# Kernel optimization log

Hardware: AMD Instinct MI355X
Metric: run time of the kernel (lower is better)

Reference implementation:

```python
import jax, jax.numpy as jnp
import numpy as np

K = 3          # spline order
NUM = 32       # grid intervals G
IN_DIM = 256
OUT_DIM = 512
BATCH = 2048


def _b_spline_basis(x, grid, k):
    """Cox-de-Boor recursion. x: (B, I); grid: (I, G+2k+1) -> (B, I, G+k)."""
    xg = x[:, :, None]                      # (B, I, 1)
    g = grid[None, :, :]                    # (1, I, G+2k+1)
    val = ((xg >= g[:, :, :-1]) & (xg < g[:, :, 1:])).astype(x.dtype)
    for p in range(1, k + 1):
        left = (xg - g[:, :, :-(p + 1)]) / (g[:, :, p:-1] - g[:, :, :-(p + 1)])
        right = (g[:, :, p + 1:] - xg) / (g[:, :, p + 1:] - g[:, :, 1:-p])
        val = left * val[:, :, :-1] + right * val[:, :, 1:]
    return val                               # (B, I, G+k)


def setup_inputs() -> dict:
    key = jax.random.key(0)
    k1, k2, k3 = jax.random.split(key, 3)
    x = jax.random.normal(k1, (BATCH, IN_DIM), dtype=jnp.float32)
    # uniform grid on [-1, 1], extended by k knots on each side (extend_grid)
    base = np.linspace(-1.0, 1.0, NUM + 1)
    h = 2.0 / NUM
    ext = np.concatenate([base[0] - h * np.arange(K, 0, -1), base,
                          base[-1] + h * np.arange(1, K + 1)]).astype(np.float32)
    grid = jnp.tile(jnp.asarray(ext)[None, :], (IN_DIM, 1))  # (I, G+2k+1)
    coef = 0.1 * jax.random.normal(k2, (IN_DIM, OUT_DIM, NUM + K), dtype=jnp.float32)
    scale_base = jax.random.normal(k3, (IN_DIM, OUT_DIM), dtype=jnp.float32) / np.sqrt(IN_DIM).astype(np.float32)
    scale_sp = jnp.ones((IN_DIM, OUT_DIM), dtype=jnp.float32) / np.sqrt(IN_DIM).astype(np.float32)
    mask = jnp.ones((IN_DIM, OUT_DIM), dtype=jnp.float32)
    return {"x": x, "grid": grid, "coef": coef,
            "scale_base": scale_base, "scale_sp": scale_sp, "mask": mask}


def reference(x, grid, coef, scale_base, scale_sp, mask):
    base = jax.nn.silu(x)                                   # b(x) residual, (B, I)
    bases = _b_spline_basis(x, grid, K)                     # (B, I, G+k)
    # coef2curve: einsum('ijk,jlk->ijl') in pykan -> (B, I, O)
    y = jnp.einsum('bik,iok->bio', bases, coef)
    y = scale_base[None, :, :] * base[:, :, None] + scale_sp[None, :, :] * y
    y = mask[None, :, :] * y
    return jnp.sum(y, axis=1)                               # (B, O)
```

## Files before the change

### kernel.cpp

```cpp
#include <hip/hip_runtime.h>
#include <math.h>

#define BATCH   2048
#define IN_DIM  256
#define OUT_DIM 512
#define NK      35
#define KS      48
#define KG      6
#define BTILE   128
#define OTILE   128
#define ICHUNK  16
#define NSPLIT  16
#define NBUF    2
#define COEFS_BYTES ((size_t)IN_DIM * OUT_DIM * KS * 2)
#define PART_ELEMS  ((size_t)BATCH * OUT_DIM)

__device__ __forceinline__ unsigned short f2bf(float x) {
    unsigned u = __float_as_uint(x);
    u += 0x7FFF + ((u >> 16) & 1);
    return (unsigned short)(u >> 16);
}
__device__ __forceinline__ float bf2f(unsigned short h) {
    return __uint_as_float(((unsigned)h) << 16);
}
__device__ __forceinline__ unsigned pack2(unsigned short a, unsigned short b) {
    return (unsigned)a | ((unsigned)b << 16);
}

typedef __bf16 bf16x8 __attribute__((ext_vector_type(8)));
typedef float  f32x16 __attribute__((ext_vector_type(16)));
typedef int    i32x4  __attribute__((ext_vector_type(4)));
typedef unsigned int u32;

__device__ __forceinline__ void gload_lds16(const void* g, void* l) {
    __builtin_amdgcn_global_load_lds((const __attribute__((address_space(1))) u32*)g,
                                     (__attribute__((address_space(3))) u32*)l, 16, 0, 0);
}

__device__ __forceinline__ unsigned lds_off(const void* p) {
    return (unsigned)(uintptr_t)(const __attribute__((address_space(3))) char*)p;
}

__device__ __forceinline__ i32x4 ds_read128(unsigned base, int off) {
    i32x4 r;
    asm volatile("ds_read_b128 %0, %1 offset:%c2"
                 : "=v"(r) : "v"(base), "i"(off));
    return r;
}
__device__ __forceinline__ bf16x8 as_bf16x8(i32x4 v) {
    bf16x8 r; __builtin_memcpy(&r, &v, 16); return r;
}

#define PR 32
__global__ __launch_bounds__(256) void kan_prep(
    const float* __restrict__ coef,
    const float* __restrict__ scale_base,
    const float* __restrict__ scale_sp,
    const float* __restrict__ mask,
    unsigned short* __restrict__ coefS)
{
    __shared__ float sc[PR * NK];
    __shared__ float sspm[PR], ssbm[PR];
    const int t    = threadIdx.x;
    const int row0 = blockIdx.x * PR;

    {
        const float4* csrc = (const float4*)(coef + (size_t)row0 * NK);
        float4* cdst = (float4*)sc;
        cdst[t] = csrc[t];
        if (t < 24) cdst[t + 256] = csrc[t + 256];
    }
    if (t < PR) {
        float m = mask[row0 + t];
        sspm[t] = scale_sp[row0 + t] * m;
        ssbm[t] = scale_base[row0 + t] * m;
    }
    __syncthreads();

    if (t < PR * 6) {
        int r = t / 6;
        int q = t - r * 6;
        float spm = sspm[r];
        const float* c = sc + r * NK;
        uint4 v = make_uint4(0u, 0u, 0u, 0u);
        if (q < 4) {
            const float* cq = c + q * 8;
            v.x = pack2(f2bf(cq[0] * spm), f2bf(cq[1] * spm));
            v.y = pack2(f2bf(cq[2] * spm), f2bf(cq[3] * spm));
            v.z = pack2(f2bf(cq[4] * spm), f2bf(cq[5] * spm));
            v.w = pack2(f2bf(cq[6] * spm), f2bf(cq[7] * spm));
        } else if (q == 4) {
            float sbm = ssbm[r];
            unsigned short hi = f2bf(sbm);
            unsigned short lo = f2bf(sbm - bf2f(hi));
            v.x = pack2(f2bf(c[32] * spm), f2bf(c[33] * spm));
            v.y = pack2(f2bf(c[34] * spm), 0);
            v.z = pack2(hi, hi);
            v.w = pack2(lo, 0);
        }
        int g = row0 + r;
        size_t di = ((size_t)(((g >> 9) * 4 + ((g >> 7) & 3)) * 6 + q)) * 128
                  + (size_t)(g & 127);
        ((uint4*)coefS)[di] = v;
    }
}

__global__ __launch_bounds__(256, 3) void kan_mfma(
    const float* __restrict__ x,
    const unsigned short* __restrict__ coefS,
    float* __restrict__ part)
{
    __shared__ __align__(16) short sA[2 * BTILE * KS];
    __shared__ __align__(16) short sB[NBUF * OTILE * KS];

    const int t    = threadIdx.x;
    const int w    = t >> 6;
    const int lane = t & 63;
    const int l31  = lane & 31, lh = lane >> 5;
    const int wr   = w & 1;
    const int wc   = w >> 1;
    const int o0   = blockIdx.x * OTILE;
    const int b0   = blockIdx.y * BTILE;
    const int ic0  = blockIdx.z * ICHUNK;
    const bool bTh = (t >= 128);
    const int wbase = t & 64;

    {
        uint4 z = make_uint4(0, 0, 0, 0);
        #pragma unroll
        for (int u = 0; u < 6; ++u) {
            int idx = t + 256 * u;
            if (idx < (2 * BTILE * KS * 2) / 16) ((uint4*)sA)[idx] = z;
        }
    }

    f32x16 acc00 = {}, acc01 = {}, acc10 = {}, acc11 = {};

    float xreg = 0.0f;
    int om0 = 0, om1 = 0;

    auto stageA = [&](short* abuf, int row, float xv, int& omn) {
        unsigned* rp = (unsigned*)abuf + row * 4;
        auto PADDR = [&](int p) -> unsigned* {
            return rp + (p >> 2) * (BTILE * 4) + (p & 3);
        };
        int oc = omn;
        *PADDR(oc)     = 0;
        *PADDR(oc + 1) = 0;
        *PADDR(oc + 2) = 0;

        float xn = (xv + 1.1875f) * 16.0f;
        float jf = floorf(xn);
        int   j  = (int)jf;
        float u  = xn - jf;
        bool valid = (xn >= 0.0f) && (j <= 37);
        float u2 = u * u, u3 = u2 * u;
        float w0 = (1.0f / 6.0f) * (1.0f - 3.0f * u + 3.0f * u2 - u3);
        float w1 = (1.0f / 6.0f) * (3.0f * u3 - 6.0f * u2 + 4.0f);
        float w2 = (1.0f / 6.0f) * (-3.0f * u3 + 3.0f * u2 + 3.0f * u + 1.0f);
        float w3 = (1.0f / 6.0f) * u3;
        int jb = j - 3;
        unsigned short h0 = f2bf(w0), h1 = f2bf(w1), h2 = f2bf(w2), h3 = f2bf(w3);
        int  m0  = jb >> 1;
        bool odd = (jb & 1) != 0;
        unsigned C0 = odd ? pack2(0, h0)
                          : (jb == 34 ? pack2(h0, 0) : pack2(h0, h1));
        unsigned C1 = odd ? (jb == 33 ? pack2(h1, 0) : pack2(h1, h2))
                          : (jb == 32 ? pack2(h2, 0) : pack2(h2, h3));
        unsigned C2 = pack2(h3, 0);
        if (valid) {
            if (m0 >= 0)                        *PADDR(m0)     = C0;
            if (m0 + 1 >= 0 && jb != 34)        *PADDR(m0 + 1) = C1;
            if (odd && jb != 33 && m0 + 2 >= 0) *PADDR(m0 + 2) = C2;
        }
        omn = min(max(m0, 0), 15);
        float sig = 1.0f / (1.0f + __expf(-xv));
        float s   = xv * sig;
        unsigned short shi = f2bf(s);
        unsigned short slo = f2bf(s - bf2f(shi));
        uint2 bw; bw.x = pack2(shi, slo); bw.y = pack2(shi, 0);
        *(uint2*)PADDR(18) = bw;
    };

    auto issueB = [&](int i, int buf) {
        const char* gsrc = (const char*)coefS
                         + ((size_t)i * 4 + (o0 >> 7)) * (KG * OTILE * 8 * 2);
        #pragma unroll
        for (int q = 0; q < 6; ++q) {
            int slot = wbase + (t & 63) + 128 * q;
            gload_lds16(gsrc + slot * 16,
                        (void*)(sB + buf * (OTILE * KS) + (wbase + 128 * q) * 8));
        }
    };

    __syncthreads();

    if (!bTh) {
        float x0 = x[(size_t)(b0 + t) * IN_DIM + ic0];
        stageA(sA, t, x0, om0);
        xreg = x[(size_t)(b0 + t) * IN_DIM + ic0 + 1];
    } else {
        issueB(ic0, 0);
    }
    if (bTh) asm volatile("s_waitcnt vmcnt(0)" ::: "memory");
    else     asm volatile("s_waitcnt lgkmcnt(0)" ::: "memory");
    __builtin_amdgcn_s_barrier();
    __builtin_amdgcn_sched_barrier(0);

    const unsigned sAoff = lds_off(sA);
    const unsigned sBoff = lds_off(sB);

    auto body = [&](int it, int& omn) {
        if (bTh && it + 1 < ICHUNK) issueB(ic0 + it + 1, (it + 1) & 1);

        const int cur = it & 1;
        const unsigned Abo = sAoff
            + (unsigned)(cur * (BTILE * KS) + (lh * BTILE + wr * 64 + l31) * 8) * 2u;
        const unsigned Bbo = sBoff
            + (unsigned)(cur * (OTILE * KS) + (lh * OTILE + wc * 64 + l31) * 8) * 2u;

        i32x4 a0r[3], a1r[3], b0r[3], b1r[3];
        #pragma unroll
        for (int s = 0; s < 3; ++s) {
            a0r[s] = ds_read128(Abo, s * 4096);
            a1r[s] = ds_read128(Abo, s * 4096 + 512);
            b0r[s] = ds_read128(Bbo, s * 4096);
            b1r[s] = ds_read128(Bbo, s * 4096 + 512);
        }

        if (!bTh && it + 1 < ICHUNK) {
            stageA(sA + ((it + 1) & 1) * (BTILE * KS), t, xreg, omn);
            if (it + 2 < ICHUNK)
                xreg = x[(size_t)(b0 + t) * IN_DIM + ic0 + it + 2];
        }

        asm volatile("s_waitcnt lgkmcnt(0)" ::: "memory");
        __builtin_amdgcn_sched_barrier(0);

        __builtin_amdgcn_s_setprio(1);
        #pragma unroll
        for (int s = 0; s < 3; ++s) {
            acc00 = __builtin_amdgcn_mfma_f32_32x32x16_bf16(as_bf16x8(a0r[s]), as_bf16x8(b0r[s]), acc00, 0, 0, 0);
            acc01 = __builtin_amdgcn_mfma_f32_32x32x16_bf16(as_bf16x8(a0r[s]), as_bf16x8(b1r[s]), acc01, 0, 0, 0);
            acc10 = __builtin_amdgcn_mfma_f32_32x32x16_bf16(as_bf16x8(a1r[s]), as_bf16x8(b0r[s]), acc10, 0, 0, 0);
            acc11 = __builtin_amdgcn_mfma_f32_32x32x16_bf16(as_bf16x8(a1r[s]), as_bf16x8(b1r[s]), acc11, 0, 0, 0);
        }
        __builtin_amdgcn_s_setprio(0);

        if (it + 1 < ICHUNK) {
            if (bTh) asm volatile("s_waitcnt vmcnt(0)" ::: "memory");
            __builtin_amdgcn_s_barrier();
            __builtin_amdgcn_sched_barrier(0);
        }
    };

    for (int itp = 0; itp < ICHUNK / 2; ++itp) {
        body(2 * itp,     om1);
        body(2 * itp + 1, om0);
    }

    __syncthreads();

    float* tp = (float*)sA + w * (32 * 36);
    float* pdst = part + (size_t)blockIdx.z * PART_ELEMS;
    #pragma unroll
    for (int r = 0; r < 2; ++r) {
        #pragma unroll
        for (int c = 0; c < 2; ++c) {
            const f32x16& acc = (r == 0) ? ((c == 0) ? acc00 : acc01)
                                         : ((c == 0) ? acc10 : acc11);
            #pragma unroll
            for (int reg = 0; reg < 16; ++reg) {
                int row = (reg & 3) + 8 * (reg >> 2) + 4 * lh;
                tp[row * 36 + l31] = acc[reg];
            }
            int cc = (lane & 7) * 4;
            #pragma unroll
            for (int j = 0; j < 4; ++j) {
                int rr = j * 8 + (lane >> 3);
                float4 v = *(float4*)&tp[rr * 36 + cc];
                int rowg = b0 + wr * 64 + r * 32 + rr;
                int colg = o0 + wc * 64 + c * 32 + cc;
                *(float4*)&pdst[(size_t)rowg * OUT_DIM + colg] = v;
            }
        }
    }
}

__global__ __launch_bounds__(256) void kan_reduce(
    const float4* __restrict__ part, float4* __restrict__ out)
{
    const size_t e = (size_t)blockIdx.x * 256 + threadIdx.x;
    float4 s = part[e];
    #pragma unroll
    for (int z = 1; z < NSPLIT; ++z) {
        float4 v = part[(size_t)z * (PART_ELEMS / 4) + e];
        s.x += v.x; s.y += v.y; s.z += v.z; s.w += v.w;
    }
    out[e] = s;
}

extern "C" void kernel_launch(void* const* d_in, const int* in_sizes, int n_in,
                              void* d_out, int out_size, void* d_ws, size_t ws_size,
                              hipStream_t stream) {
    const float* x          = (const float*)d_in[0];
    const float* coef       = (const float*)d_in[2];
    const float* scale_base = (const float*)d_in[3];
    const float* scale_sp   = (const float*)d_in[4];
    const float* mask       = (const float*)d_in[5];
    unsigned short* coefS   = (unsigned short*)d_ws;
    float* part             = (float*)((char*)d_ws + COEFS_BYTES);

    kan_prep<<<dim3(IN_DIM * OUT_DIM / PR), dim3(256), 0, stream>>>(
        coef, scale_base, scale_sp, mask, coefS);
    kan_mfma<<<dim3(OUT_DIM / OTILE, BATCH / BTILE, NSPLIT), dim3(256), 0, stream>>>(
        x, coefS, part);
    kan_reduce<<<dim3(BATCH * OUT_DIM / 4 / 256), dim3(256), 0, stream>>>(
        (const float4*)part, (float4*)d_out);
}
```

Baseline: 131.3 us.

## Precompute spline basis in prep kernel and deepen coef prefetch pipeline

Moves per-element B-spline weight and SiLU computation out of the MFMA kernel into the prep kernel, which writes packed basis words and bf16 hi/lo SiLU values to workspace. The MFMA kernel now only loads these and scatters them into LDS. It also raises the coefficient buffer count to four, prefetches three stages ahead with a partial vmcnt wait, and doubles the input-chunk length while halving the split count. In exchange it adds 24 bytes of workspace traffic per x element, uses more LDS, and lowers the occupancy bound from three to two blocks.

```diff
diff --git a/kernel.cpp b/kernel.cpp
--- a/kernel.cpp
+++ b/kernel.cpp
@@ -9,11 +9,13 @@
 #define KG      6
 #define BTILE   128
 #define OTILE   128
-#define ICHUNK  16
-#define NSPLIT  16
-#define NBUF    2
+#define ICHUNK  32
+#define NSPLIT  8
+#define NBUF    4
 #define COEFS_BYTES ((size_t)IN_DIM * OUT_DIM * KS * 2)
 #define PART_ELEMS  ((size_t)BATCH * OUT_DIM)
+#define XP4_OFF (COEFS_BYTES + (size_t)NSPLIT * PART_ELEMS * 4)
+#define XP2_OFF (XP4_OFF + (size_t)BATCH * IN_DIM * 16)
 
 __device__ __forceinline__ unsigned short f2bf(float x) {
     unsigned u = __float_as_uint(x);
@@ -53,11 +55,14 @@
 
 #define PR 32
 __global__ __launch_bounds__(256) void kan_prep(
+    const float* __restrict__ x,
     const float* __restrict__ coef,
     const float* __restrict__ scale_base,
     const float* __restrict__ scale_sp,
     const float* __restrict__ mask,
-    unsigned short* __restrict__ coefS)
+    unsigned short* __restrict__ coefS,
+    uint4* __restrict__ xp4,
+    uint2* __restrict__ xp2)
 {
     __shared__ float sc[PR * NK];
     __shared__ float sspm[PR], ssbm[PR];
@@ -74,6 +79,44 @@
         float m = mask[row0 + t];
         sspm[t] = scale_sp[row0 + t] * m;
         ssbm[t] = scale_base[row0 + t] * m;
+    }
+
+    if (blockIdx.x < (BATCH * IN_DIM) / 256) {
+        int flat = blockIdx.x * 256 + t;
+        float xv = x[flat];
+        float xn = (xv + 1.1875f) * 16.0f;
+        float jf = floorf(xn);
+        int   j  = (int)jf;
+        float u  = xn - jf;
+        bool valid = (xn >= 0.0f) && (j <= 37);
+        float u2 = u * u, u3 = u2 * u;
+        float w0 = (1.0f / 6.0f) * (1.0f - 3.0f * u + 3.0f * u2 - u3);
+        float w1 = (1.0f / 6.0f) * (3.0f * u3 - 6.0f * u2 + 4.0f);
+        float w2 = (1.0f / 6.0f) * (-3.0f * u3 + 3.0f * u2 + 3.0f * u + 1.0f);
+        float w3f = (1.0f / 6.0f) * u3;
+        int jb = j - 3;
+        unsigned short h0 = f2bf(w0), h1 = f2bf(w1), h2 = f2bf(w2), h3 = f2bf(w3f);
+        int  m0  = jb >> 1;
+        bool odd = (jb & 1) != 0;
+        unsigned C0 = odd ? pack2(0, h0)
+                          : (jb == 34 ? pack2(h0, 0) : pack2(h0, h1));
+        unsigned C1 = odd ? (jb == 33 ? pack2(h1, 0) : pack2(h1, h2))
+                          : (jb == 32 ? pack2(h2, 0) : pack2(h2, h3));
+        unsigned C2 = pack2(h3, 0);
+        int e0 = (valid && (m0 >= 0)) ? 1 : 0;
+        int e1 = (valid && (m0 + 1 >= 0) && (jb != 34)) ? 1 : 0;
+        int e2 = (valid && odd && (jb != 33) && (m0 + 2 >= 0)) ? 1 : 0;
+        int sat = min(max(m0, -2), 17);
+        uint4 c;
+        c.x = C0; c.y = C1; c.z = C2;
+        c.w = (unsigned)((sat + 2) | (e0 << 8) | (e1 << 9) | (e2 << 10));
+        float sig = 1.0f / (1.0f + __expf(-xv));
+        float s   = xv * sig;
+        unsigned short shi = f2bf(s);
+        unsigned short slo = f2bf(s - bf2f(shi));
+        uint2 bw; bw.x = pack2(shi, slo); bw.y = pack2(shi, 0);
+        xp4[flat] = c;
+        xp2[flat] = bw;
     }
     __syncthreads();
 
@@ -105,8 +148,10 @@
     }
 }
 
-__global__ __launch_bounds__(256, 3) void kan_mfma(
+__global__ __launch_bounds__(256, 2) void kan_mfma(
     const float* __restrict__ x,
+    const uint4* __restrict__ xp4,
+    const uint2* __restrict__ xp2,
     const unsigned short* __restrict__ coefS,
     float* __restrict__ part)
 {
@@ -136,10 +181,11 @@
 
     f32x16 acc00 = {}, acc01 = {}, acc10 = {}, acc11 = {};
 
-    float xreg = 0.0f;
     int om0 = 0, om1 = 0;
-
-    auto stageA = [&](short* abuf, int row, float xv, int& omn) {
+    uint4 cA = make_uint4(0, 0, 0, 0);
+    uint2 bA = make_uint2(0, 0);
+
+    auto stageA = [&](short* abuf, int row, uint4 c, uint2 bw, int& omn) {
         unsigned* rp = (unsigned*)abuf + row * 4;
         auto PADDR = [&](int p) -> unsigned* {
             return rp + (p >> 2) * (BTILE * 4) + (p & 3);
@@ -148,37 +194,12 @@
         *PADDR(oc)     = 0;
         *PADDR(oc + 1) = 0;
         *PADDR(oc + 2) = 0;
-
-        float xn = (xv + 1.1875f) * 16.0f;
-        float jf = floorf(xn);
-        int   j  = (int)jf;
-        float u  = xn - jf;
-        bool valid = (xn >= 0.0f) && (j <= 37);
-        float u2 = u * u, u3 = u2 * u;
-        float w0 = (1.0f / 6.0f) * (1.0f - 3.0f * u + 3.0f * u2 - u3);
-        float w1 = (1.0f / 6.0f) * (3.0f * u3 - 6.0f * u2 + 4.0f);
-        float w2 = (1.0f / 6.0f) * (-3.0f * u3 + 3.0f * u2 + 3.0f * u + 1.0f);
-        float w3 = (1.0f / 6.0f) * u3;
-        int jb = j - 3;
-        unsigned short h0 = f2bf(w0), h1 = f2bf(w1), h2 = f2bf(w2), h3 = f2bf(w3);
-        int  m0  = jb >> 1;
-        bool odd = (jb & 1) != 0;
-        unsigned C0 = odd ? pack2(0, h0)
-                          : (jb == 34 ? pack2(h0, 0) : pack2(h0, h1));
-        unsigned C1 = odd ? (jb == 33 ? pack2(h1, 0) : pack2(h1, h2))
-                          : (jb == 32 ? pack2(h2, 0) : pack2(h2, h3));
-        unsigned C2 = pack2(h3, 0);
-        if (valid) {
-            if (m0 >= 0)                        *PADDR(m0)     = C0;
-            if (m0 + 1 >= 0 && jb != 34)        *PADDR(m0 + 1) = C1;
-            if (odd && jb != 33 && m0 + 2 >= 0) *PADDR(m0 + 2) = C2;
-        }
+        int w3 = (int)c.w;
+        int m0 = (w3 & 255) - 2;
+        if (w3 & 256)  *PADDR(m0)     = c.x;
+        if (w3 & 512)  *PADDR(m0 + 1) = c.y;
+        if (w3 & 1024) *PADDR(m0 + 2) = c.z;
         omn = min(max(m0, 0), 15);
-        float sig = 1.0f / (1.0f + __expf(-xv));
-        float s   = xv * sig;
-        unsigned short shi = f2bf(s);
-        unsigned short slo = f2bf(s - bf2f(shi));
-        uint2 bw; bw.x = pack2(shi, slo); bw.y = pack2(shi, 0);
         *(uint2*)PADDR(18) = bw;
     };
 
@@ -196,13 +217,18 @@
     __syncthreads();
 
     if (!bTh) {
-        float x0 = x[(size_t)(b0 + t) * IN_DIM + ic0];
-        stageA(sA, t, x0, om0);
-        xreg = x[(size_t)(b0 + t) * IN_DIM + ic0 + 1];
+        size_t xbase = (size_t)(b0 + t) * IN_DIM + ic0;
+        uint4 c0 = xp4[xbase];
+        uint2 b0v = xp2[xbase];
+        stageA(sA, t, c0, b0v, om0);
+        cA = xp4[xbase + 1];
+        bA = xp2[xbase + 1];
     } else {
-        issueB(ic0, 0);
-    }
-    if (bTh) asm volatile("s_waitcnt vmcnt(0)" ::: "memory");
+        issueB(ic0,     0);
+        issueB(ic0 + 1, 1);
+        issueB(ic0 + 2, 2);
+    }
+    if (bTh) asm volatile("s_waitcnt vmcnt(12)" ::: "memory");
     else     asm volatile("s_waitcnt lgkmcnt(0)" ::: "memory");
     __builtin_amdgcn_s_barrier();
     __builtin_amdgcn_sched_barrier(0);
@@ -211,13 +237,17 @@
     const unsigned sBoff = lds_off(sB);
 
     auto body = [&](int it, int& omn) {
-        if (bTh && it + 1 < ICHUNK) issueB(ic0 + it + 1, (it + 1) & 1);
+        if (bTh && it + 1 < ICHUNK) {
+            int ip3 = (it + 3 < ICHUNK) ? (it + 3) : (ICHUNK - 1);
+            issueB(ic0 + ip3, (it + 3) & (NBUF - 1));
+        }
 
         const int cur = it & 1;
         const unsigned Abo = sAoff
             + (unsigned)(cur * (BTILE * KS) + (lh * BTILE + wr * 64 + l31) * 8) * 2u;
         const unsigned Bbo = sBoff
-            + (unsigned)(cur * (OTILE * KS) + (lh * OTILE + wc * 64 + l31) * 8) * 2u;
+            + (unsigned)((it & (NBUF - 1)) * (OTILE * KS)
+                         + (lh * OTILE + wc * 64 + l31) * 8) * 2u;
 
         i32x4 a0r[3], a1r[3], b0r[3], b1r[3];
         #pragma unroll
@@ -229,9 +259,12 @@
         }
 
         if (!bTh && it + 1 < ICHUNK) {
-            stageA(sA + ((it + 1) & 1) * (BTILE * KS), t, xreg, omn);
-            if (it + 2 < ICHUNK)
-                xreg = x[(size_t)(b0 + t) * IN_DIM + ic0 + it + 2];
+            stageA(sA + ((it + 1) & 1) * (BTILE * KS), t, cA, bA, omn);
+            if (it + 2 < ICHUNK) {
+                size_t xbase = (size_t)(b0 + t) * IN_DIM + ic0 + it + 2;
+                cA = xp4[xbase];
+                bA = xp2[xbase];
+            }
         }
 
         asm volatile("s_waitcnt lgkmcnt(0)" ::: "memory");
@@ -248,7 +281,8 @@
         __builtin_amdgcn_s_setprio(0);
 
         if (it + 1 < ICHUNK) {
-            if (bTh) asm volatile("s_waitcnt vmcnt(0)" ::: "memory");
+            if (bTh) asm volatile("s_waitcnt vmcnt(12)" ::: "memory");
+            else     asm volatile("s_waitcnt lgkmcnt(0)" ::: "memory");
             __builtin_amdgcn_s_barrier();
             __builtin_amdgcn_sched_barrier(0);
         }
@@ -310,11 +344,13 @@
     const float* mask       = (const float*)d_in[5];
     unsigned short* coefS   = (unsigned short*)d_ws;
     float* part             = (float*)((char*)d_ws + COEFS_BYTES);
+    uint4* xp4              = (uint4*)((char*)d_ws + XP4_OFF);
+    uint2* xp2              = (uint2*)((char*)d_ws + XP2_OFF);
 
     kan_prep<<<dim3(IN_DIM * OUT_DIM / PR), dim3(256), 0, stream>>>(
-        coef, scale_base, scale_sp, mask, coefS);
+        x, coef, scale_base, scale_sp, mask, coefS, xp4, xp2);
     kan_mfma<<<dim3(OUT_DIM / OTILE, BATCH / BTILE, NSPLIT), dim3(256), 0, stream>>>(
-        x, coefS, part);
+        x, xp4, xp2, coefS, part);
     kan_reduce<<<dim3(BATCH * OUT_DIM / 4 / 256), dim3(256), 0, stream>>>(
         (const float4*)part, (float4*)d_out);
 }
```

New measurement: 123.0 us. -6.3%, faster.
